# Optimization experiments

Hardware: AMD Instinct MI355X
Metric: run time of the kernel (lower is better)

Reference implementation:

```python
import jax, jax.numpy as jnp
import numpy as np

N = 100000      # nodes
E = 1600000     # edges (avg degree 16)
IN, H, H4, OUT = 2, 128, 32, 64
B = 1000        # batch_size for final view


def setup_inputs() -> dict:
    key = jax.random.key(0)
    ks = jax.random.split(key, 16)
    w = lambda k, s: (jax.random.normal(k, s, jnp.float32) * (1.0 / np.sqrt(s[0])))
    return {
        "x": jax.random.normal(ks[0], (N, IN), jnp.float32),
        "edge_index": jax.random.randint(ks[1], (2, E), 0, N, dtype=jnp.int32),
        "batch_size": B,
        "W1": w(ks[2], (IN, H)),  "b1": jnp.zeros((H,), jnp.float32),
        "W2": w(ks[3], (H, H)),   "b2": jnp.zeros((H,), jnp.float32),
        "W3": w(ks[4], (H, H4)),  "b3": jnp.zeros((H4,), jnp.float32),
        "W4": w(ks[5], (H4, H4)), "b4": jnp.zeros((H4,), jnp.float32),
        "W5": w(ks[6], (H4, OUT)),"b5": jnp.zeros((OUT,), jnp.float32),
        "Wl": w(ks[7], (OUT, 1)), "bl": jnp.zeros((1,), jnp.float32),
    }


def gcn_conv(x, src, dst, W, b, n):
    # PyG GCNConv: add self-loops, symmetric degree normalization, scatter-add.
    h = x @ W  # [N, F]
    deg = jax.ops.segment_sum(jnp.ones(src.shape[0], h.dtype), dst,
                              num_segments=n) + 1.0  # +1 for self-loop
    dinv = jax.lax.rsqrt(deg)  # deg >= 1, no inf
    norm = dinv[src] * dinv[dst]  # [E]
    agg = jax.ops.segment_sum(h[src] * norm[:, None], dst, num_segments=n)
    agg = agg + h * (dinv * dinv)[:, None]  # self-loop contribution
    return agg + b


def reference(x, edge_index, batch_size, W1, b1, W2, b2, W3, b3, W4, b4, W5, b5, Wl, bl):
    x = x.reshape(-1, 2)
    n = x.shape[0]
    src, dst = edge_index[0], edge_index[1]
    for W, b in ((W1, b1), (W2, b2), (W3, b3), (W4, b4), (W5, b5)):
        x = jax.nn.relu(gcn_conv(x, src, dst, W, b, n))
    x = x @ Wl + bl  # [N, 1]
    return x.reshape(batch_size, -1)
```

## Files before the change

### kernel.cpp

```cpp
#include <hip/hip_runtime.h>
#include <math.h>


static inline int cdiv(int a, int b) { return (a + b - 1) / b; }

__global__ void zero_i32(int* __restrict__ p, int n) {
    int i = blockIdx.x * 256 + threadIdx.x;
    if (i < n) p[i] = 0;
}

__global__ __launch_bounds__(256) void count_ranged(const int* __restrict__ dst,
                                                    int* __restrict__ cnt,
                                                    int E, int N, int echunk) {
    int cls = blockIdx.x & 7;
    int chunk = blockIdx.x >> 3;
    int per = (N + 7) >> 3;
    int lo = cls * per;
    int hi = lo + per; if (hi > N) hi = N;
    int e0 = chunk * echunk;
    int e1 = e0 + echunk; if (e1 > E) e1 = E;
    for (int e = e0 + (int)threadIdx.x; e < e1; e += 256) {
        int d = dst[e];
        if (d >= lo && d < hi) atomicAdd(&cnt[d], 1);
    }
}

__global__ void scan1(const int* __restrict__ cnt, int* __restrict__ off,
                      int* __restrict__ bsum, int n) {
    __shared__ int sm[256];
    int i = blockIdx.x * 256 + threadIdx.x;
    int v = (i < n) ? cnt[i] : 0;
    sm[threadIdx.x] = v;
    __syncthreads();
    for (int ofs = 1; ofs < 256; ofs <<= 1) {
        int t = (threadIdx.x >= (unsigned)ofs) ? sm[threadIdx.x - ofs] : 0;
        __syncthreads();
        sm[threadIdx.x] += t;
        __syncthreads();
    }
    if (i < n) off[i] = sm[threadIdx.x];
    if (threadIdx.x == 255) bsum[blockIdx.x] = sm[255];
}

__global__ void scan2(const int* __restrict__ bsum, int* __restrict__ bpre,
                      int nb, int* __restrict__ off, int N, int E) {
    __shared__ int sm[512];
    int t = threadIdx.x;
    sm[t] = (t < nb) ? bsum[t] : 0;
    __syncthreads();
    for (int ofs = 1; ofs < 512; ofs <<= 1) {
        int v = (t >= ofs) ? sm[t - ofs] : 0;
        __syncthreads();
        sm[t] += v;
        __syncthreads();
    }
    if (t < nb) bpre[t] = sm[t] - bsum[t];
    if (t == 0) off[N] = E;
}

__global__ void scan3_fused(const int* __restrict__ cnt, const int* __restrict__ bpre,
                            int* __restrict__ off, int* __restrict__ cursor,
                            const float* __restrict__ x, float* __restrict__ dinv,
                            float* __restrict__ xs, int n) {
    int i = blockIdx.x * 256 + threadIdx.x;
    if (i < n) {
        int c = cnt[i];
        int o = off[i] - c + bpre[blockIdx.x];
        off[i] = o;
        cursor[i] = o;
        float dv = 1.0f / sqrtf((float)c + 1.0f);
        dinv[i] = dv;
        float2 xv = *reinterpret_cast<const float2*>(x + 2 * (size_t)i);
        *reinterpret_cast<float2*>(xs + 2 * (size_t)i) = float2{dv * xv.x, dv * xv.y};
    }
}

__global__ __launch_bounds__(256) void fill_ranged(const int* __restrict__ src,
                                                   const int* __restrict__ dst,
                                                   int* __restrict__ cursor,
                                                   int* __restrict__ csr,
                                                   int E, int N, int echunk) {
    int cls = blockIdx.x & 7;
    int chunk = blockIdx.x >> 3;
    int per = (N + 7) >> 3;
    int lo = cls * per;
    int hi = lo + per; if (hi > N) hi = N;
    int e0 = chunk * echunk;
    int e1 = e0 + echunk; if (e1 > E) e1 = E;
    for (int e = e0 + (int)threadIdx.x; e < e1; e += 256) {
        int d = dst[e];
        if (d >= lo && d < hi) {
            int p = atomicAdd(&cursor[d], 1);
            csr[p] = src[e];
        }
    }
}

__global__ __launch_bounds__(256) void agg2_kernel(const float* __restrict__ xs,
                                                   const int* __restrict__ off,
                                                   const int* __restrict__ csr,
                                                   const float* __restrict__ dinv,
                                                   float* __restrict__ out, int n) {
    int v = blockIdx.x * 256 + threadIdx.x;
    if (v >= n) return;
    float a0 = 0.f, a1 = 0.f;
    int e0 = off[v], e1 = off[v + 1];
    for (int e = e0; e < e1; e++) {
        int s = csr[e];
        float2 q = *reinterpret_cast<const float2*>(xs + 2 * (size_t)s);
        a0 += q.x;
        a1 += q.y;
    }
    float dv = dinv[v];
    float2 xv = *reinterpret_cast<const float2*>(xs + 2 * (size_t)v);
    *reinterpret_cast<float2*>(out + 2 * (size_t)v) =
        float2{dv * (a0 + xv.x), dv * (a1 + xv.y)};
}

template <bool BR, bool PS>
__global__ __launch_bounds__(256) void agg128_kernel(const float* __restrict__ h,
                                                     const int* __restrict__ off,
                                                     const int* __restrict__ csr,
                                                     const float* __restrict__ dinv,
                                                     const float* __restrict__ bias,
                                                     float* __restrict__ out, int n) {
    int tid = threadIdx.x;
    int lane = tid & 63;
    int sl = lane & 15;
    int subbase = lane & ~15;
    int wave = tid >> 6;
    int v = blockIdx.x * 16 + wave * 4 + (lane >> 4);
    if (v >= n) return;

    int start = off[v];
    int end = off[v + 1];

    float4 accA = {0.f, 0.f, 0.f, 0.f};
    float4 accB = {0.f, 0.f, 0.f, 0.f};

    for (int base = start; base < end; base += 16) {
        int m = end - base;
        if (m > 16) m = 16;
        int idx = (sl < m) ? csr[base + sl] : 0;
        int i = 0;
        for (; i + 8 <= m; i += 8) {
            float4 ha[8], hb[8];
#pragma unroll
            for (int u = 0; u < 8; u++) {
                int s = __shfl(idx, subbase + i + u);
                const float* p = h + (size_t)s * 128 + sl * 8;
                ha[u] = *reinterpret_cast<const float4*>(p);
                hb[u] = *reinterpret_cast<const float4*>(p + 4);
            }
#pragma unroll
            for (int u = 0; u < 8; u++) {
                accA.x += ha[u].x; accA.y += ha[u].y; accA.z += ha[u].z; accA.w += ha[u].w;
                accB.x += hb[u].x; accB.y += hb[u].y; accB.z += hb[u].z; accB.w += hb[u].w;
            }
        }
        if (i + 4 <= m) {
            float4 ha[4], hb[4];
#pragma unroll
            for (int u = 0; u < 4; u++) {
                int s = __shfl(idx, subbase + i + u);
                const float* p = h + (size_t)s * 128 + sl * 8;
                ha[u] = *reinterpret_cast<const float4*>(p);
                hb[u] = *reinterpret_cast<const float4*>(p + 4);
            }
#pragma unroll
            for (int u = 0; u < 4; u++) {
                accA.x += ha[u].x; accA.y += ha[u].y; accA.z += ha[u].z; accA.w += ha[u].w;
                accB.x += hb[u].x; accB.y += hb[u].y; accB.z += hb[u].z; accB.w += hb[u].w;
            }
            i += 4;
        }
        if (i + 2 <= m) {
            int s0 = __shfl(idx, subbase + i);
            int s1 = __shfl(idx, subbase + i + 1);
            const float* p0 = h + (size_t)s0 * 128 + sl * 8;
            const float* p1 = h + (size_t)s1 * 128 + sl * 8;
            float4 a0 = *reinterpret_cast<const float4*>(p0);
            float4 b0 = *reinterpret_cast<const float4*>(p0 + 4);
            float4 a1 = *reinterpret_cast<const float4*>(p1);
            float4 b1 = *reinterpret_cast<const float4*>(p1 + 4);
            accA.x += a0.x + a1.x; accA.y += a0.y + a1.y;
            accA.z += a0.z + a1.z; accA.w += a0.w + a1.w;
            accB.x += b0.x + b1.x; accB.y += b0.y + b1.y;
            accB.z += b0.z + b1.z; accB.w += b0.w + b1.w;
            i += 2;
        }
        if (i < m) {
            int s0 = __shfl(idx, subbase + i);
            const float* p0 = h + (size_t)s0 * 128 + sl * 8;
            float4 a0 = *reinterpret_cast<const float4*>(p0);
            float4 b0 = *reinterpret_cast<const float4*>(p0 + 4);
            accA.x += a0.x; accA.y += a0.y; accA.z += a0.z; accA.w += a0.w;
            accB.x += b0.x; accB.y += b0.y; accB.z += b0.z; accB.w += b0.w;
        }
    }

    float dv = dinv[v];
    const float* pv = h + (size_t)v * 128 + sl * 8;
    float4 hvA = *reinterpret_cast<const float4*>(pv);
    float4 hvB = *reinterpret_cast<const float4*>(pv + 4);
    float4 oA, oB;
    oA.x = dv * (accA.x + hvA.x); oA.y = dv * (accA.y + hvA.y);
    oA.z = dv * (accA.z + hvA.z); oA.w = dv * (accA.w + hvA.w);
    oB.x = dv * (accB.x + hvB.x); oB.y = dv * (accB.y + hvB.y);
    oB.z = dv * (accB.z + hvB.z); oB.w = dv * (accB.w + hvB.w);
    if constexpr (BR) {
        float4 bA = *reinterpret_cast<const float4*>(bias + sl * 8);
        float4 bB = *reinterpret_cast<const float4*>(bias + sl * 8 + 4);
        oA.x = fmaxf(oA.x + bA.x, 0.f); oA.y = fmaxf(oA.y + bA.y, 0.f);
        oA.z = fmaxf(oA.z + bA.z, 0.f); oA.w = fmaxf(oA.w + bA.w, 0.f);
        oB.x = fmaxf(oB.x + bB.x, 0.f); oB.y = fmaxf(oB.y + bB.y, 0.f);
        oB.z = fmaxf(oB.z + bB.z, 0.f); oB.w = fmaxf(oB.w + bB.w, 0.f);
    }
    if constexpr (PS) {
        oA.x *= dv; oA.y *= dv; oA.z *= dv; oA.w *= dv;
        oB.x *= dv; oB.y *= dv; oB.z *= dv; oB.w *= dv;
    }
    float* po = out + (size_t)v * 128 + sl * 8;
    *reinterpret_cast<float4*>(po) = oA;
    *reinterpret_cast<float4*>(po + 4) = oB;
}

template <bool BR, bool PS>
__global__ __launch_bounds__(256) void agg32_kernel(const float* __restrict__ h,
                                                    const int* __restrict__ off,
                                                    const int* __restrict__ csr,
                                                    const float* __restrict__ dinv,
                                                    const float* __restrict__ bias,
                                                    float* __restrict__ out, int n) {
    int tid = threadIdx.x;
    int lane = tid & 63;
    int sl = lane & 7;
    int subbase = lane & ~7;
    int wave = tid >> 6;
    int v = blockIdx.x * 32 + wave * 8 + (lane >> 3);
    if (v >= n) return;

    int start = off[v];
    int end = off[v + 1];

    float4 acc = {0.f, 0.f, 0.f, 0.f};

    for (int base = start; base < end; base += 16) {
        int m = end - base;
        if (m > 16) m = 16;
        int idxA = (sl < m) ? csr[base + sl] : 0;
        int idxB = (8 + sl < m) ? csr[base + 8 + sl] : 0;
        if (m == 16) {
            float4 hb[16];
#pragma unroll
            for (int u = 0; u < 16; u++) {
                int s = __shfl((u < 8) ? idxA : idxB, subbase + (u & 7));
                hb[u] = *reinterpret_cast<const float4*>(h + (size_t)s * 32 + sl * 4);
            }
#pragma unroll
            for (int u = 0; u < 16; u++) {
                acc.x += hb[u].x; acc.y += hb[u].y; acc.z += hb[u].z; acc.w += hb[u].w;
            }
        } else {
            int ma = (m < 8) ? m : 8;
            int i = 0;
            for (; i + 4 <= ma; i += 4) {
                float4 hb[4];
#pragma unroll
                for (int u = 0; u < 4; u++) {
                    int s = __shfl(idxA, subbase + i + u);
                    hb[u] = *reinterpret_cast<const float4*>(h + (size_t)s * 32 + sl * 4);
                }
#pragma unroll
                for (int u = 0; u < 4; u++) {
                    acc.x += hb[u].x; acc.y += hb[u].y; acc.z += hb[u].z; acc.w += hb[u].w;
                }
            }
            if (i + 2 <= ma) {
                int s0 = __shfl(idxA, subbase + i);
                int s1 = __shfl(idxA, subbase + i + 1);
                float4 h0 = *reinterpret_cast<const float4*>(h + (size_t)s0 * 32 + sl * 4);
                float4 h1 = *reinterpret_cast<const float4*>(h + (size_t)s1 * 32 + sl * 4);
                acc.x += h0.x + h1.x; acc.y += h0.y + h1.y;
                acc.z += h0.z + h1.z; acc.w += h0.w + h1.w;
                i += 2;
            }
            if (i < ma) {
                int s0 = __shfl(idxA, subbase + i);
                float4 h0 = *reinterpret_cast<const float4*>(h + (size_t)s0 * 32 + sl * 4);
                acc.x += h0.x; acc.y += h0.y; acc.z += h0.z; acc.w += h0.w;
            }
            if (m > 8) {
                int mb = m - 8;
                int j = 0;
                for (; j + 4 <= mb; j += 4) {
                    float4 hb[4];
#pragma unroll
                    for (int u = 0; u < 4; u++) {
                        int s = __shfl(idxB, subbase + j + u);
                        hb[u] = *reinterpret_cast<const float4*>(h + (size_t)s * 32 + sl * 4);
                    }
#pragma unroll
                    for (int u = 0; u < 4; u++) {
                        acc.x += hb[u].x; acc.y += hb[u].y; acc.z += hb[u].z; acc.w += hb[u].w;
                    }
                }
                if (j + 2 <= mb) {
                    int s0 = __shfl(idxB, subbase + j);
                    int s1 = __shfl(idxB, subbase + j + 1);
                    float4 h0 = *reinterpret_cast<const float4*>(h + (size_t)s0 * 32 + sl * 4);
                    float4 h1 = *reinterpret_cast<const float4*>(h + (size_t)s1 * 32 + sl * 4);
                    acc.x += h0.x + h1.x; acc.y += h0.y + h1.y;
                    acc.z += h0.z + h1.z; acc.w += h0.w + h1.w;
                    j += 2;
                }
                if (j < mb) {
                    int s0 = __shfl(idxB, subbase + j);
                    float4 h0 = *reinterpret_cast<const float4*>(h + (size_t)s0 * 32 + sl * 4);
                    acc.x += h0.x; acc.y += h0.y; acc.z += h0.z; acc.w += h0.w;
                }
            }
        }
    }

    float dv = dinv[v];
    float4 hv = *reinterpret_cast<const float4*>(h + (size_t)v * 32 + sl * 4);
    float o0 = dv * (acc.x + hv.x);
    float o1 = dv * (acc.y + hv.y);
    float o2 = dv * (acc.z + hv.z);
    float o3 = dv * (acc.w + hv.w);
    if constexpr (BR) {
        float4 b = *reinterpret_cast<const float4*>(bias + sl * 4);
        o0 = fmaxf(o0 + b.x, 0.f);
        o1 = fmaxf(o1 + b.y, 0.f);
        o2 = fmaxf(o2 + b.z, 0.f);
        o3 = fmaxf(o3 + b.w, 0.f);
    }
    if constexpr (PS) {
        o0 *= dv; o1 *= dv; o2 *= dv; o3 *= dv;
    }
    *reinterpret_cast<float4*>(out + (size_t)v * 32 + sl * 4) = float4{o0, o1, o2, o3};
}

template <int K, int F, bool BR, bool PS>
__global__ __launch_bounds__(256, 4) void gemm_tiled(const float* __restrict__ x,
                                                     const float* __restrict__ W,
                                                     const float* __restrict__ bias,
                                                     const float* __restrict__ dinv,
                                                     float* __restrict__ h, int n) {
    constexpr int KC = 16;
    constexpr int KCP = 20;
    constexpr int ROWS = 64;
    constexpr int TPC = F / 4;
    constexpr int RT = 256 / TPC;
    constexpr int RPT = ROWS / RT;
    static_assert(K % KC == 0, "K must be a multiple of 16");

    __shared__ float Ws[KC * F];
    __shared__ float Xs[ROWS * KCP];

    const int tid = threadIdx.x;
    const int cb = (tid % TPC) * 4;
    const int tr = tid / TPC;
    const int row0 = blockIdx.x * ROWS;

    float acc[RPT][4];
#pragma unroll
    for (int r = 0; r < RPT; r++)
#pragma unroll
        for (int j = 0; j < 4; j++) acc[r][j] = 0.f;

#pragma unroll 1
    for (int k0 = 0; k0 < K; k0 += KC) {
        __syncthreads();
        {
            int r = tid >> 2;
            int kk = (tid & 3) * 4;
            int gr = row0 + r;
            float4 v = (gr < n)
                ? *reinterpret_cast<const float4*>(x + (size_t)gr * K + k0 + kk)
                : float4{0.f, 0.f, 0.f, 0.f};
            *reinterpret_cast<float4*>(&Xs[r * KCP + kk]) = v;
        }
        for (int i = tid; i < KC * F / 4; i += 256) {
            *reinterpret_cast<float4*>(&Ws[i * 4]) =
                *reinterpret_cast<const float4*>(W + (size_t)k0 * F + i * 4);
        }
        __syncthreads();

#pragma unroll
        for (int kk4 = 0; kk4 < KC; kk4 += 4) {
            float4 xr[RPT];
#pragma unroll
            for (int r = 0; r < RPT; r++)
                xr[r] = *reinterpret_cast<const float4*>(&Xs[(tr * RPT + r) * KCP + kk4]);
#pragma unroll
            for (int j = 0; j < 4; j++) {
                float4 w = *reinterpret_cast<const float4*>(&Ws[(kk4 + j) * F + cb]);
#pragma unroll
                for (int r = 0; r < RPT; r++) {
                    float xv = (j == 0) ? xr[r].x : (j == 1) ? xr[r].y
                             : (j == 2) ? xr[r].z : xr[r].w;
                    acc[r][0] += xv * w.x;
                    acc[r][1] += xv * w.y;
                    acc[r][2] += xv * w.z;
                    acc[r][3] += xv * w.w;
                }
            }
        }
    }

    float4 b = float4{0.f, 0.f, 0.f, 0.f};
    if constexpr (BR) b = *reinterpret_cast<const float4*>(bias + cb);
#pragma unroll
    for (int r = 0; r < RPT; r++) {
        int row = row0 + tr * RPT + r;
        if (row < n) {
            float o0 = acc[r][0], o1 = acc[r][1], o2 = acc[r][2], o3 = acc[r][3];
            if constexpr (BR) {
                o0 = fmaxf(o0 + b.x, 0.f);
                o1 = fmaxf(o1 + b.y, 0.f);
                o2 = fmaxf(o2 + b.z, 0.f);
                o3 = fmaxf(o3 + b.w, 0.f);
            }
            if constexpr (PS) {
                float dv = dinv[row];
                o0 *= dv; o1 *= dv; o2 *= dv; o3 *= dv;
            }
            *reinterpret_cast<float4*>(&h[(size_t)row * F + cb]) = float4{o0, o1, o2, o3};
        }
    }
}

template <int K, int F, bool BR, bool PS>
__global__ __launch_bounds__(256, 4) void gemm_small(const float* __restrict__ x,
                                                     const float* __restrict__ W,
                                                     const float* __restrict__ bias,
                                                     const float* __restrict__ dinv,
                                                     float* __restrict__ h, int n) {
    constexpr int TPR = F / 4;
    constexpr int ROWS = 256 / TPR;
    __shared__ float Ws[K * F];
    for (int i = threadIdx.x; i < K * F; i += 256) Ws[i] = W[i];
    __syncthreads();

    int tid = threadIdx.x;
    int cb = (tid % TPR) * 4;
    int r = blockIdx.x * ROWS + tid / TPR;
    if (r >= n) return;

    const float* xr = x + (size_t)r * K;
    float a0 = 0.f, a1 = 0.f, a2 = 0.f, a3 = 0.f;
#pragma unroll
    for (int k = 0; k < K; k++) {
        float xv = xr[k];
        float4 w = *reinterpret_cast<const float4*>(&Ws[k * F + cb]);
        a0 += xv * w.x; a1 += xv * w.y; a2 += xv * w.z; a3 += xv * w.w;
    }
    if constexpr (BR) {
        float4 b = *reinterpret_cast<const float4*>(bias + cb);
        a0 = fmaxf(a0 + b.x, 0.f);
        a1 = fmaxf(a1 + b.y, 0.f);
        a2 = fmaxf(a2 + b.z, 0.f);
        a3 = fmaxf(a3 + b.w, 0.f);
    }
    if constexpr (PS) {
        float dv = dinv[r];
        a0 *= dv; a1 *= dv; a2 *= dv; a3 *= dv;
    }
    *reinterpret_cast<float4*>(&h[(size_t)r * F + cb]) = float4{a0, a1, a2, a3};
}

__global__ __launch_bounds__(256) void final_kernel(const float* __restrict__ x,
                                                    const float* __restrict__ Wl,
                                                    const float* __restrict__ bl,
                                                    float* __restrict__ out, int n) {
    __shared__ float w[64];
    if (threadIdx.x < 64) w[threadIdx.x] = Wl[threadIdx.x];
    __syncthreads();
    int i = blockIdx.x * 256 + threadIdx.x;
    if (i >= n) return;
    const float* r = x + (size_t)i * 64;
    float acc = 0.f;
#pragma unroll
    for (int k = 0; k < 64; k += 4) {
        float4 xv = *reinterpret_cast<const float4*>(r + k);
        acc += xv.x * w[k] + xv.y * w[k + 1] + xv.z * w[k + 2] + xv.w * w[k + 3];
    }
    out[i] = acc + bl[0];
}

extern "C" void kernel_launch(void* const* d_in, const int* in_sizes, int n_in,
                              void* d_out, int out_size, void* d_ws, size_t ws_size,
                              hipStream_t stream) {
    const float* x = (const float*)d_in[0];
    const int* ei = (const int*)d_in[1];
    const float* W1 = (const float*)d_in[3];
    const float* b1 = (const float*)d_in[4];
    const float* W2 = (const float*)d_in[5];
    const float* b2 = (const float*)d_in[6];
    const float* W3 = (const float*)d_in[7];
    const float* b3 = (const float*)d_in[8];
    const float* W4 = (const float*)d_in[9];
    const float* b4 = (const float*)d_in[10];
    const float* W5 = (const float*)d_in[11];
    const float* b5 = (const float*)d_in[12];
    const float* Wl = (const float*)d_in[13];
    const float* bl = (const float*)d_in[14];

    const int N = in_sizes[0] / 2;
    const int E = in_sizes[1] / 2;
    const int* src = ei;
    const int* dst = ei + E;

    char* wp = (char*)d_ws;
    auto alloc = [&](size_t bytes) -> void* {
        void* p = wp;
        wp += ((bytes + 255) / 256) * 256;
        return p;
    };
    int* cnt = (int*)alloc((size_t)N * 4);
    int* off = (int*)alloc((size_t)(N + 1) * 4);
    int* cursor = (int*)alloc((size_t)N * 4);
    int* bsum = (int*)alloc(512 * 4);
    int* bpre = (int*)alloc(512 * 4);
    int* csr = (int*)alloc((size_t)E * 4);
    float* dinv = (float*)alloc((size_t)N * 4);
    float* xs2 = (float*)alloc((size_t)N * 2 * 4);
    float* t2 = (float*)alloc((size_t)N * 2 * 4);
    float* bufA = (float*)alloc((size_t)N * 128 * 4);
    float* bufB = (float*)alloc((size_t)N * 128 * 4);

    const int gN = cdiv(N, 256);
    const int nb = gN;
    const int gT = cdiv(N, 64);

    const int NCHUNK = 128;
    const int echunk = cdiv(E, NCHUNK);
    const int gR = 8 * NCHUNK;

    zero_i32<<<gN, 256, 0, stream>>>(cnt, N);
    count_ranged<<<gR, 256, 0, stream>>>(dst, cnt, E, N, echunk);
    scan1<<<nb, 256, 0, stream>>>(cnt, off, bsum, N);
    scan2<<<1, 512, 0, stream>>>(bsum, bpre, nb, off, N, E);
    scan3_fused<<<nb, 256, 0, stream>>>(cnt, bpre, off, cursor, x, dinv, xs2, N);
    fill_ranged<<<gR, 256, 0, stream>>>(src, dst, cursor, csr, E, N, echunk);

    agg2_kernel<<<gN, 256, 0, stream>>>(xs2, off, csr, dinv, t2, N);
    gemm_small<2, 128, true, true><<<cdiv(N, 8), 256, 0, stream>>>(t2, W1, b1, dinv, bufA, N);
    gemm_tiled<128, 128, false, false><<<gT, 256, 0, stream>>>(bufA, W2, nullptr, nullptr, bufB, N);
    agg128_kernel<true, true><<<cdiv(N, 16), 256, 0, stream>>>(bufB, off, csr, dinv, b2, bufA, N);
    gemm_tiled<128, 32, false, false><<<gT, 256, 0, stream>>>(bufA, W3, nullptr, nullptr, bufB, N);
    agg32_kernel<true, true><<<cdiv(N, 32), 256, 0, stream>>>(bufB, off, csr, dinv, b3, bufA, N);
    gemm_tiled<32, 32, false, false><<<gT, 256, 0, stream>>>(bufA, W4, nullptr, nullptr, bufB, N);
    agg32_kernel<true, true><<<cdiv(N, 32), 256, 0, stream>>>(bufB, off, csr, dinv, b4, bufA, N);
    agg32_kernel<false, false><<<cdiv(N, 32), 256, 0, stream>>>(bufA, off, csr, dinv, nullptr, bufB, N);
    gemm_tiled<32, 64, true, false><<<gT, 256, 0, stream>>>(bufB, W5, b5, nullptr, bufA, N);
    final_kernel<<<gN, 256, 0, stream>>>(bufA, Wl, bl, (float*)d_out, N);
}
```

Baseline: 573.8 us.

## Pre-bucket edges by destination class before CSR count and fill

Replaces the range-filtered count and fill passes, which each read every edge eight times, with a two-level bucketing scheme. Edges are first counted per destination class and scattered into class buckets that pack src and local dst into one word, then count and fill operate per class on compact bucket ranges. This cuts redundant global reads of the edge list and keeps atomics localised per class, at the cost of extra kernels, an extra E-sized buffer, and a packing scheme that requires src and local dst bits to fit in 32 bits.

Measured after the change: 596.4 us. 1.04x slower.

```diff
diff --git a/kernel.cpp b/kernel.cpp
--- a/kernel.cpp
+++ b/kernel.cpp
@@ -9,19 +9,85 @@
     if (i < n) p[i] = 0;
 }
 
-__global__ __launch_bounds__(256) void count_ranged(const int* __restrict__ dst,
-                                                    int* __restrict__ cnt,
-                                                    int E, int N, int echunk) {
+__global__ __launch_bounds__(256) void class_count(const int* __restrict__ dst,
+                                                   int* __restrict__ bcls,
+                                                   int E, int per) {
+    __shared__ int lc[8];
+    int t = threadIdx.x;
+    if (t < 8) lc[t] = 0;
+    __syncthreads();
+    for (int e = blockIdx.x * 256 + t; e < E; e += gridDim.x * 256) {
+        atomicAdd(&lc[dst[e] / per], 1);
+    }
+    __syncthreads();
+    if (t < 8) atomicAdd(&bcls[t], lc[t]);
+}
+
+__global__ void class_scan(const int* __restrict__ bcls, int* __restrict__ cbase,
+                           int* __restrict__ bcur) {
+    if (threadIdx.x == 0) {
+        int s = 0;
+        for (int c = 0; c < 8; c++) {
+            cbase[c] = s;
+            bcur[c] = s;
+            s += bcls[c];
+        }
+        cbase[8] = s;
+    }
+}
+
+__global__ __launch_bounds__(256) void bucket_scatter(const int* __restrict__ src,
+                                                      const int* __restrict__ dst,
+                                                      int* __restrict__ bcur,
+                                                      unsigned int* __restrict__ buckets,
+                                                      int E, int per, int shift) {
+    __shared__ int lcnt[8], lbase[8], lpos[8];
+    int t = threadIdx.x;
+    if (t < 8) lcnt[t] = 0;
+    __syncthreads();
+
+    int e0 = blockIdx.x * 2048;
+    int sv[8], dv[8], cv[8];
+#pragma unroll
+    for (int u = 0; u < 8; u++) {
+        int e = e0 + u * 256 + t;
+        if (e < E) {
+            sv[u] = src[e];
+            dv[u] = dst[e];
+            cv[u] = dv[u] / per;
+            atomicAdd(&lcnt[cv[u]], 1);
+        } else {
+            cv[u] = -1;
+        }
+    }
+    __syncthreads();
+    if (t < 8) {
+        lbase[t] = atomicAdd(&bcur[t], lcnt[t]);
+        lpos[t] = 0;
+    }
+    __syncthreads();
+#pragma unroll
+    for (int u = 0; u < 8; u++) {
+        if (cv[u] >= 0) {
+            int p = atomicAdd(&lpos[cv[u]], 1);
+            buckets[lbase[cv[u]] + p] =
+                ((unsigned int)sv[u] << shift) | (unsigned int)(dv[u] - cv[u] * per);
+        }
+    }
+}
+
+__global__ __launch_bounds__(256) void count_local(const unsigned int* __restrict__ buckets,
+                                                   const int* __restrict__ cbase,
+                                                   int* __restrict__ cnt,
+                                                   int per, int shift) {
     int cls = blockIdx.x & 7;
     int chunk = blockIdx.x >> 3;
-    int per = (N + 7) >> 3;
+    int nch = gridDim.x >> 3;
+    int b0 = cbase[cls], b1 = cbase[cls + 1];
+    unsigned int mask = (1u << shift) - 1u;
     int lo = cls * per;
-    int hi = lo + per; if (hi > N) hi = N;
-    int e0 = chunk * echunk;
-    int e1 = e0 + echunk; if (e1 > E) e1 = E;
-    for (int e = e0 + (int)threadIdx.x; e < e1; e += 256) {
-        int d = dst[e];
-        if (d >= lo && d < hi) atomicAdd(&cnt[d], 1);
+    for (int i = b0 + chunk * 256 + (int)threadIdx.x; i < b1; i += nch * 256) {
+        atomicAdd(&cnt[lo + (int)(buckets[i] & mask)], 1);
     }
 }
 
@@ -75,24 +141,23 @@
     }
 }
 
-__global__ __launch_bounds__(256) void fill_ranged(const int* __restrict__ src,
-                                                   const int* __restrict__ dst,
-                                                   int* __restrict__ cursor,
-                                                   int* __restrict__ csr,
-                                                   int E, int N, int echunk) {
+__global__ __launch_bounds__(256) void fill_local(const unsigned int* __restrict__ buckets,
+                                                  const int* __restrict__ cbase,
+                                                  int* __restrict__ cursor,
+                                                  int* __restrict__ csr,
+                                                  int per, int shift) {
     int cls = blockIdx.x & 7;
     int chunk = blockIdx.x >> 3;
-    int per = (N + 7) >> 3;
+    int nch = gridDim.x >> 3;
+    int b0 = cbase[cls], b1 = cbase[cls + 1];
+    unsigned int mask = (1u << shift) - 1u;
     int lo = cls * per;
-    int hi = lo + per; if (hi > N) hi = N;
-    int e0 = chunk * echunk;
-    int e1 = e0 + echunk; if (e1 > E) e1 = E;
-    for (int e = e0 + (int)threadIdx.x; e < e1; e += 256) {
-        int d = dst[e];
-        if (d >= lo && d < hi) {
-            int p = atomicAdd(&cursor[d], 1);
-            csr[p] = src[e];
-        }
+    for (int i = b0 + chunk * 256 + (int)threadIdx.x; i < b1; i += nch * 256) {
+        unsigned int ent = buckets[i];
+        int d = lo + (int)(ent & mask);
+        int s = (int)(ent >> shift);
+        int p = atomicAdd(&cursor[d], 1);
+        csr[p] = s;
     }
 }
 
@@ -525,6 +590,10 @@
     int* bsum = (int*)alloc(512 * 4);
     int* bpre = (int*)alloc(512 * 4);
     int* csr = (int*)alloc((size_t)E * 4);
+    unsigned int* buckets = (unsigned int*)alloc((size_t)E * 4);
+    int* bcls = (int*)alloc(16 * 4);
+    int* cbase = (int*)alloc(16 * 4);
+    int* bcur = (int*)alloc(16 * 4);
     float* dinv = (float*)alloc((size_t)N * 4);
     float* xs2 = (float*)alloc((size_t)N * 2 * 4);
     float* t2 = (float*)alloc((size_t)N * 2 * 4);
@@ -535,16 +604,20 @@
     const int nb = gN;
     const int gT = cdiv(N, 64);
 
-    const int NCHUNK = 128;
-    const int echunk = cdiv(E, NCHUNK);
-    const int gR = 8 * NCHUNK;
+    const int per = (N + 7) / 8;
+    int shift = 0;
+    while ((1 << shift) < per) shift++;
 
     zero_i32<<<gN, 256, 0, stream>>>(cnt, N);
-    count_ranged<<<gR, 256, 0, stream>>>(dst, cnt, E, N, echunk);
+    zero_i32<<<1, 256, 0, stream>>>(bcls, 16);
+    class_count<<<256, 256, 0, stream>>>(dst, bcls, E, per);
+    class_scan<<<1, 64, 0, stream>>>(bcls, cbase, bcur);
+    bucket_scatter<<<cdiv(E, 2048), 256, 0, stream>>>(src, dst, bcur, buckets, E, per, shift);
+    count_local<<<256, 256, 0, stream>>>(buckets, cbase, cnt, per, shift);
     scan1<<<nb, 256, 0, stream>>>(cnt, off, bsum, N);
     scan2<<<1, 512, 0, stream>>>(bsum, bpre, nb, off, N, E);
     scan3_fused<<<nb, 256, 0, stream>>>(cnt, bpre, off, cursor, x, dinv, xs2, N);
-    fill_ranged<<<gR, 256, 0, stream>>>(src, dst, cursor, csr, E, N, echunk);
+    fill_local<<<256, 256, 0, stream>>>(buckets, cbase, cursor, csr, per, shift);
 
     agg2_kernel<<<gN, 256, 0, stream>>>(xs2, off, csr, dinv, t2, N);
     gemm_small<2, 128, true, true><<<cdiv(N, 8), 256, 0, stream>>>(t2, W1, b1, dinv, bufA, N);
```
